# Optimization experiments

Measured on AMD Instinct MI355X. Metric: run time of the kernel, lower is better.

## Reference

```python
import jax, jax.numpy as jnp
import numpy as np

B, D, E, H, C = 2048, 1024, 8, 4096, 1024
TOP_K = 2
LN_EPS = 1e-5


def setup_inputs() -> dict:
    key = jax.random.key(0)
    ks = jax.random.split(key, 5)
    x = jax.random.normal(ks[0], (B, D), dtype=jnp.float32)
    Wr = jax.random.normal(ks[1], (D, E), dtype=jnp.float32) * 0.02
    br = jnp.zeros((E,), dtype=jnp.float32)
    ln_g = jnp.ones((E, D), dtype=jnp.float32)
    ln_b = jnp.zeros((E, D), dtype=jnp.float32)
    W1 = jax.random.normal(ks[2], (E, D, H), dtype=jnp.float32) * 0.02
    b1 = jnp.zeros((E, H), dtype=jnp.float32)
    W2 = jax.random.normal(ks[3], (E, H, C), dtype=jnp.float32) * 0.02
    b2 = jnp.zeros((E, C), dtype=jnp.float32)
    return {"x": x, "Wr": Wr, "br": br, "ln_g": ln_g, "ln_b": ln_b,
            "W1": W1, "b1": b1, "W2": W2, "b2": b2}


def reference(x, Wr, br, ln_g, ln_b, W1, b1, W2, b2):
    # Router (eval mode: no jitter)
    router_logits = x @ Wr + br                       # [B, E]
    topk_vals, topk_idx = jax.lax.top_k(router_logits, TOP_K)
    topk_w = jax.nn.softmax(topk_vals, axis=-1)       # [B, K]
    # Scatter top-k weights into a dense [B, E] combine matrix (indices unique per row)
    w_full = jnp.zeros((x.shape[0], E), dtype=x.dtype)
    w_full = w_full.at[jnp.arange(x.shape[0])[:, None], topk_idx].set(topk_w)
    # Shared LayerNorm statistics, per-expert affine
    mu = jnp.mean(x, axis=-1, keepdims=True)
    var = jnp.mean(jnp.square(x - mu), axis=-1, keepdims=True)
    xn = (x - mu) * jax.lax.rsqrt(var + LN_EPS)       # [B, D]
    xe = xn[:, None, :] * ln_g[None] + ln_b[None]     # [B, E, D]
    # Expert MLPs (dense over experts; combine weights zero-out non-selected experts)
    h = jax.nn.gelu(jnp.einsum('bed,edh->beh', xe, W1) + b1[None], approximate=False)
    y = jnp.einsum('beh,ehc->bec', h, W2) + b2[None]  # [B, E, C]
    out = jnp.einsum('be,bec->bc', w_full, y)         # weighted combine
    return out
```

## Files before the change

kernel.cpp:

```cpp
#include <hip/hip_runtime.h>
#include <hip/hip_bf16.h>

#define B_TOK 2048
#define D_DIM 1024
#define E_NUM 8
#define H_DIM 4096
#define C_DIM 1024
#define CAP   5120
#define MAXT  40

typedef __attribute__((ext_vector_type(8))) short bf16x8;
typedef __attribute__((ext_vector_type(4))) float floatx4;

__device__ __forceinline__ unsigned short f2bf(float f) {
  union { float f; unsigned int u; } a; a.f = f;
  unsigned int u = a.u;
  return (unsigned short)((u + 0x7FFFu + ((u >> 16) & 1u)) >> 16);
}

__device__ __forceinline__ void gload_lds16(const void* g, void* l) {
  __builtin_amdgcn_global_load_lds(
      (const __attribute__((address_space(1))) void*)g,
      (__attribute__((address_space(3))) void*)l, 16, 0, 0);
}

__global__ void kinit(int* counts) {
  if (threadIdx.x < E_NUM) counts[threadIdx.x] = 0;
}

__global__ __launch_bounds__(256) void krouter(const float* __restrict__ x,
                                               const float* __restrict__ Wr,
                                               const float* __restrict__ br,
                                               int2* meta_i, float4* meta_f, int* counts) {
  int b = blockIdx.x, t = threadIdx.x;
  const float4 xv = *(const float4*)(x + (size_t)b * D_DIM + t * 4);
  float v[10];
  v[0] = xv.x + xv.y + xv.z + xv.w;
  v[1] = xv.x * xv.x + xv.y * xv.y + xv.z * xv.z + xv.w * xv.w;
#pragma unroll
  for (int e = 0; e < 8; e++) v[2 + e] = 0.f;
  const float* wr = Wr + (size_t)(t * 4) * E_NUM;
  float xs[4] = {xv.x, xv.y, xv.z, xv.w};
#pragma unroll
  for (int j = 0; j < 4; j++) {
    float4 wa = *(const float4*)(wr + j * 8);
    float4 wb = *(const float4*)(wr + j * 8 + 4);
    v[2] += xs[j] * wa.x; v[3] += xs[j] * wa.y; v[4] += xs[j] * wa.z; v[5] += xs[j] * wa.w;
    v[6] += xs[j] * wb.x; v[7] += xs[j] * wb.y; v[8] += xs[j] * wb.z; v[9] += xs[j] * wb.w;
  }
#pragma unroll
  for (int i = 0; i < 10; i++) {
    float s = v[i];
#pragma unroll
    for (int off = 32; off > 0; off >>= 1) s += __shfl_down(s, off, 64);
    v[i] = s;
  }
  __shared__ float red[4][10];
  int lane = t & 63, wid = t >> 6;
  if (lane == 0) {
#pragma unroll
    for (int i = 0; i < 10; i++) red[wid][i] = v[i];
  }
  __syncthreads();
  if (t == 0) {
    float f[10];
#pragma unroll
    for (int i = 0; i < 10; i++) f[i] = red[0][i] + red[1][i] + red[2][i] + red[3][i];
    float mu = f[0] * (1.f / 1024.f);
    float var = f[1] * (1.f / 1024.f) - mu * mu;
    float rsig = rsqrtf(var + 1e-5f);
    float lg[8];
#pragma unroll
    for (int e = 0; e < 8; e++) lg[e] = f[2 + e] + br[e];
    int i0 = 0;
#pragma unroll
    for (int e = 1; e < 8; e++) if (lg[e] > lg[i0]) i0 = e;
    int i1 = (i0 == 0) ? 1 : 0;
#pragma unroll
    for (int e = 0; e < 8; e++) if (e != i0 && lg[e] > lg[i1]) i1 = e;
    float ex = expf(lg[i1] - lg[i0]);
    float w0 = 1.f / (1.f + ex);
    float w1 = 1.f - w0;
    atomicAdd(counts + i0, 1);
    atomicAdd(counts + i1, 1);
    meta_i[b] = make_int2(i0, i1);
    meta_f[b] = make_float4(w0, w1, mu, rsig);
  }
}

__global__ void kprefix(const int* counts, int* cursor, int* tmap_e, int* tmap_r) {
  if (threadIdx.x == 0) {
    int total = 0, tt = 0;
    for (int e = 0; e < E_NUM; e++) {
      cursor[e] = total;
      int nt = (counts[e] + 127) >> 7;
      for (int i = 0; i < nt; i++) { tmap_e[tt] = e; tmap_r[tt] = total + i * 128; tt++; }
      total += nt << 7;
    }
    for (; tt < MAXT; tt++) tmap_e[tt] = -1;
  }
}

__global__ __launch_bounds__(256) void kscatter(const float* __restrict__ x,
                                                const float* __restrict__ ln_g,
                                                const float* __restrict__ ln_b,
                                                const int2* __restrict__ meta_i,
                                                const float4* __restrict__ meta_f,
                                                int* cursor, int2* meta_s,
                                                unsigned short* __restrict__ xe) {
  int b = blockIdx.x, t = threadIdx.x;
  __shared__ int se[2], ss[2];
  __shared__ float smu, srs;
  if (t == 0) {
    int2 mi = meta_i[b];
    float4 mf = meta_f[b];
    int s0 = atomicAdd(cursor + mi.x, 1);
    int s1 = atomicAdd(cursor + mi.y, 1);
    meta_s[b] = make_int2(s0, s1);
    se[0] = mi.x; se[1] = mi.y; ss[0] = s0; ss[1] = s1;
    smu = mf.z; srs = mf.w;
  }
  __syncthreads();
  int i = t * 4;
  float4 xv = *(const float4*)(x + (size_t)b * D_DIM + i);
  float mu = smu, rs = srs;
  float xn0 = (xv.x - mu) * rs, xn1 = (xv.y - mu) * rs, xn2 = (xv.z - mu) * rs, xn3 = (xv.w - mu) * rs;
#pragma unroll
  for (int k = 0; k < 2; k++) {
    int e = se[k], s = ss[k];
    float4 g = *(const float4*)(ln_g + (size_t)e * D_DIM + i);
    float4 bb = *(const float4*)(ln_b + (size_t)e * D_DIM + i);
    union { unsigned short us[4]; uint2 v; } u;
    u.us[0] = f2bf(xn0 * g.x + bb.x);
    u.us[1] = f2bf(xn1 * g.y + bb.y);
    u.us[2] = f2bf(xn2 * g.z + bb.z);
    u.us[3] = f2bf(xn3 * g.w + bb.w);
    *(uint2*)(xe + (size_t)s * D_DIM + i) = u.v;
  }
}

__global__ __launch_bounds__(256) void ktranspose(const float* __restrict__ src,
                                                  unsigned short* __restrict__ dst,
                                                  int R, int C) {
  __shared__ float tile[64][65];
  int z = blockIdx.z;
  const float* s = src + (size_t)z * R * C;
  unsigned short* d = dst + (size_t)z * R * C;
  int cx = blockIdx.x * 64, ry = blockIdx.y * 64;
  int t = threadIdx.x;
  int cl4 = (t & 15) * 4, rl = t >> 4;
#pragma unroll
  for (int p = 0; p < 4; p++) {
    int r = rl + p * 16;
    float4 v = *(const float4*)(s + (size_t)(ry + r) * C + cx + cl4);
    tile[r][cl4] = v.x; tile[r][cl4 + 1] = v.y; tile[r][cl4 + 2] = v.z; tile[r][cl4 + 3] = v.w;
  }
  __syncthreads();
#pragma unroll
  for (int p = 0; p < 4; p++) {
    int c = rl + p * 16;
    union { unsigned short us[4]; uint2 v; } u;
    u.us[0] = f2bf(tile[cl4][c]);
    u.us[1] = f2bf(tile[cl4 + 1][c]);
    u.us[2] = f2bf(tile[cl4 + 2][c]);
    u.us[3] = f2bf(tile[cl4 + 3][c]);
    *(uint2*)(d + (size_t)(cx + c) * R + ry + cl4) = u.v;
  }
}

__global__ __launch_bounds__(256) void kgemm1(const unsigned short* __restrict__ xe,
                                              const unsigned short* __restrict__ w1t,
                                              const float* __restrict__ b1,
                                              unsigned short* __restrict__ h,
                                              const int* __restrict__ tmap_e,
                                              const int* __restrict__ tmap_r) {
  int e = tmap_e[blockIdx.y];
  if (e < 0) return;
  int row0 = tmap_r[blockIdx.y];
  int n0 = blockIdx.x * 128;
  const unsigned short* Ab = xe + (size_t)row0 * D_DIM;
  const unsigned short* Bb = w1t + (size_t)e * H_DIM * D_DIM + (size_t)n0 * D_DIM;
  __shared__ unsigned short As[128 * 32];
  __shared__ unsigned short Bs[128 * 32];
  int t = threadIdx.x, lane = t & 63, wid = t >> 6;
  int c0 = wid * 2, c1 = c0 + 1;
  int lr0 = c0 * 16 + (lane >> 2);
  int kc = (lane & 3) * 8;
  const unsigned short* ga0 = Ab + (size_t)lr0 * D_DIM + kc;
  const unsigned short* ga1 = ga0 + 16 * D_DIM;
  const unsigned short* gb0 = Bb + (size_t)lr0 * D_DIM + kc;
  const unsigned short* gb1 = gb0 + 16 * D_DIM;
  unsigned short* la0 = As + c0 * 512;
  unsigned short* la1 = As + c1 * 512;
  unsigned short* lb0 = Bs + c0 * 512;
  unsigned short* lb1 = Bs + c1 * 512;
  int l15 = lane & 15, q = lane >> 4;
  int wm = (wid & 1) * 64, wn = (wid >> 1) * 64;
  const unsigned short* pa[4];
  const unsigned short* pb[4];
#pragma unroll
  for (int i = 0; i < 4; i++) {
    pa[i] = As + (wm + i * 16 + l15) * 32 + q * 8;
    pb[i] = Bs + (wn + i * 16 + l15) * 32 + q * 8;
  }
  floatx4 acc[4][4];
#pragma unroll
  for (int i = 0; i < 4; i++)
#pragma unroll
    for (int j = 0; j < 4; j++) acc[i][j] = (floatx4){0.f, 0.f, 0.f, 0.f};

  for (int k0 = 0; k0 < D_DIM; k0 += 32) {
    gload_lds16(ga0, la0);
    gload_lds16(ga1, la1);
    gload_lds16(gb0, lb0);
    gload_lds16(gb1, lb1);
    __syncthreads();
    bf16x8 af[4], bfr[4];
#pragma unroll
    for (int i = 0; i < 4; i++) { af[i] = *(const bf16x8*)pa[i]; bfr[i] = *(const bf16x8*)pb[i]; }
#pragma unroll
    for (int mt = 0; mt < 4; mt++)
#pragma unroll
      for (int nt = 0; nt < 4; nt++)
        acc[mt][nt] = __builtin_amdgcn_mfma_f32_16x16x32_bf16(af[mt], bfr[nt], acc[mt][nt], 0, 0, 0);
    __syncthreads();
    ga0 += 32; ga1 += 32; gb0 += 32; gb1 += 32;
  }
  float b1v[4];
#pragma unroll
  for (int nt = 0; nt < 4; nt++) b1v[nt] = b1[(size_t)e * H_DIM + n0 + wn + nt * 16 + l15];
#pragma unroll
  for (int mt = 0; mt < 4; mt++) {
    int row = row0 + wm + mt * 16 + q * 4;
#pragma unroll
    for (int nt = 0; nt < 4; nt++) {
      int col = n0 + wn + nt * 16 + l15;
      unsigned short* hp = h + (size_t)row * H_DIM + col;
#pragma unroll
      for (int r = 0; r < 4; r++) {
        float v = acc[mt][nt][r] + b1v[nt];
        v = 0.5f * v * (1.f + erff(v * 0.70710678118f));
        hp[(size_t)r * H_DIM] = f2bf(v);
      }
    }
  }
}

__global__ __launch_bounds__(256) void kgemm2(const unsigned short* __restrict__ h,
                                              const unsigned short* __restrict__ w2t,
                                              float* __restrict__ ypart,
                                              const int* __restrict__ tmap_e,
                                              const int* __restrict__ tmap_r) {
  int e = tmap_e[blockIdx.y];
  if (e < 0) return;
  int row0 = tmap_r[blockIdx.y];
  int n0 = blockIdx.x * 128;
  int kz = blockIdx.z;
  const unsigned short* Ab = h + (size_t)row0 * H_DIM + kz * 2048;
  const unsigned short* Bb = w2t + (size_t)e * C_DIM * H_DIM + (size_t)n0 * H_DIM + kz * 2048;
  float* yo = ypart + (size_t)kz * CAP * C_DIM;
  __shared__ unsigned short As[128 * 32];
  __shared__ unsigned short Bs[128 * 32];
  int t = threadIdx.x, lane = t & 63, wid = t >> 6;
  int c0 = wid * 2, c1 = c0 + 1;
  int lr0 = c0 * 16 + (lane >> 2);
  int kc = (lane & 3) * 8;
  const unsigned short* ga0 = Ab + (size_t)lr0 * H_DIM + kc;
  const unsigned short* ga1 = ga0 + (size_t)16 * H_DIM;
  const unsigned short* gb0 = Bb + (size_t)lr0 * H_DIM + kc;
  const unsigned short* gb1 = gb0 + (size_t)16 * H_DIM;
  unsigned short* la0 = As + c0 * 512;
  unsigned short* la1 = As + c1 * 512;
  unsigned short* lb0 = Bs + c0 * 512;
  unsigned short* lb1 = Bs + c1 * 512;
  int l15 = lane & 15, q = lane >> 4;
  int wm = (wid & 1) * 64, wn = (wid >> 1) * 64;
  const unsigned short* pa[4];
  const unsigned short* pb[4];
#pragma unroll
  for (int i = 0; i < 4; i++) {
    pa[i] = As + (wm + i * 16 + l15) * 32 + q * 8;
    pb[i] = Bs + (wn + i * 16 + l15) * 32 + q * 8;
  }
  floatx4 acc[4][4];
#pragma unroll
  for (int i = 0; i < 4; i++)
#pragma unroll
    for (int j = 0; j < 4; j++) acc[i][j] = (floatx4){0.f, 0.f, 0.f, 0.f};

  for (int k0 = 0; k0 < 2048; k0 += 32) {
    gload_lds16(ga0, la0);
    gload_lds16(ga1, la1);
    gload_lds16(gb0, lb0);
    gload_lds16(gb1, lb1);
    __syncthreads();
    bf16x8 af[4], bfr[4];
#pragma unroll
    for (int i = 0; i < 4; i++) { af[i] = *(const bf16x8*)pa[i]; bfr[i] = *(const bf16x8*)pb[i]; }
#pragma unroll
    for (int mt = 0; mt < 4; mt++)
#pragma unroll
      for (int nt = 0; nt < 4; nt++)
        acc[mt][nt] = __builtin_amdgcn_mfma_f32_16x16x32_bf16(af[mt], bfr[nt], acc[mt][nt], 0, 0, 0);
    __syncthreads();
    ga0 += 32; ga1 += 32; gb0 += 32; gb1 += 32;
  }
#pragma unroll
  for (int mt = 0; mt < 4; mt++) {
    int rbase = row0 + wm + mt * 16 + q * 4;
#pragma unroll
    for (int nt = 0; nt < 4; nt++) {
      int col = n0 + wn + nt * 16 + l15;
#pragma unroll
      for (int r = 0; r < 4; r++)
        yo[(size_t)(rbase + r) * C_DIM + col] = acc[mt][nt][r];
    }
  }
}

__global__ __launch_bounds__(256) void kfinal(const float* __restrict__ ypart,
                                              const int2* __restrict__ meta_i,
                                              const int2* __restrict__ meta_s,
                                              const float4* __restrict__ meta_f,
                                              const float* __restrict__ b2,
                                              float* __restrict__ out) {
  int b = blockIdx.x, t = threadIdx.x;
  int i = t * 4;
  int2 mi = meta_i[b];
  int2 ms = meta_s[b];
  float4 mf = meta_f[b];
  const float* y0 = ypart;
  const float* y1 = ypart + (size_t)CAP * C_DIM;
  float4 a0 = *(const float4*)(y0 + (size_t)ms.x * C_DIM + i);
  float4 a1 = *(const float4*)(y1 + (size_t)ms.x * C_DIM + i);
  float4 c0 = *(const float4*)(y0 + (size_t)ms.y * C_DIM + i);
  float4 c1 = *(const float4*)(y1 + (size_t)ms.y * C_DIM + i);
  float4 p = *(const float4*)(b2 + (size_t)mi.x * C_DIM + i);
  float4 qv = *(const float4*)(b2 + (size_t)mi.y * C_DIM + i);
  float4 o;
  o.x = mf.x * (a0.x + a1.x + p.x) + mf.y * (c0.x + c1.x + qv.x);
  o.y = mf.x * (a0.y + a1.y + p.y) + mf.y * (c0.y + c1.y + qv.y);
  o.z = mf.x * (a0.z + a1.z + p.z) + mf.y * (c0.z + c1.z + qv.z);
  o.w = mf.x * (a0.w + a1.w + p.w) + mf.y * (c0.w + c1.w + qv.w);
  *(float4*)(out + (size_t)b * C_DIM + i) = o;
}

extern "C" void kernel_launch(void* const* d_in, const int* in_sizes, int n_in,
                              void* d_out, int out_size, void* d_ws, size_t ws_size,
                              hipStream_t stream) {
  const float* x    = (const float*)d_in[0];
  const float* Wr   = (const float*)d_in[1];
  const float* br   = (const float*)d_in[2];
  const float* ln_g = (const float*)d_in[3];
  const float* ln_b = (const float*)d_in[4];
  const float* W1   = (const float*)d_in[5];
  const float* b1   = (const float*)d_in[6];
  const float* W2   = (const float*)d_in[7];
  const float* b2   = (const float*)d_in[8];

  char* w = (char*)d_ws;
  auto alloc = [&](size_t sz) { char* p = w; w += (sz + 255) & ~(size_t)255; return p; };
  unsigned short* W1t = (unsigned short*)alloc((size_t)E_NUM * H_DIM * D_DIM * 2);
  unsigned short* W2t = (unsigned short*)alloc((size_t)E_NUM * C_DIM * H_DIM * 2);
  unsigned short* xe  = (unsigned short*)alloc((size_t)CAP * D_DIM * 2);
  unsigned short* hb  = (unsigned short*)alloc((size_t)CAP * H_DIM * 2);
  float* ypart        = (float*)alloc((size_t)2 * CAP * C_DIM * 4);
  int2* meta_i        = (int2*)alloc((size_t)B_TOK * 8);
  int2* meta_s        = (int2*)alloc((size_t)B_TOK * 8);
  float4* meta_f      = (float4*)alloc((size_t)B_TOK * 16);
  int* counts         = (int*)alloc(64);
  int* cursor         = (int*)alloc(64);
  int* tmap_e         = (int*)alloc(MAXT * 4);
  int* tmap_r         = (int*)alloc(MAXT * 4);

  hipLaunchKernelGGL(ktranspose, dim3(H_DIM / 64, D_DIM / 64, E_NUM), dim3(256), 0, stream,
                     W1, W1t, D_DIM, H_DIM);
  hipLaunchKernelGGL(ktranspose, dim3(C_DIM / 64, H_DIM / 64, E_NUM), dim3(256), 0, stream,
                     W2, W2t, H_DIM, C_DIM);
  hipLaunchKernelGGL(kinit, dim3(1), dim3(64), 0, stream, counts);
  hipLaunchKernelGGL(krouter, dim3(B_TOK), dim3(256), 0, stream,
                     x, Wr, br, meta_i, meta_f, counts);
  hipLaunchKernelGGL(kprefix, dim3(1), dim3(64), 0, stream,
                     counts, cursor, tmap_e, tmap_r);
  hipLaunchKernelGGL(kscatter, dim3(B_TOK), dim3(256), 0, stream,
                     x, ln_g, ln_b, meta_i, meta_f, cursor, meta_s, xe);
  hipLaunchKernelGGL(kgemm1, dim3(H_DIM / 128, MAXT), dim3(256), 0, stream,
                     xe, W1t, b1, hb, tmap_e, tmap_r);
  hipLaunchKernelGGL(kgemm2, dim3(C_DIM / 128, MAXT, 2), dim3(256), 0, stream,
                     hb, W2t, ypart, tmap_e, tmap_r);
  hipLaunchKernelGGL(kfinal, dim3(B_TOK), dim3(256), 0, stream,
                     ypart, meta_i, meta_s, meta_f, b2, (float*)d_out);
}
```

Before: 584.4 us.

## Double-buffer LDS tiles with BK=64 in both expert GEMM kernels

Both expert GEMM kernels now use a two-stage LDS ping-pong buffer with a 64-wide K tile instead of a single 32-wide tile. The next tile's global-to-LDS loads are issued right after one barrier per iteration, so they overlap with the MFMA work on the current tile. This removes the second barrier and halves the number of loop iterations. In exchange, LDS use per block grows to 64 KB, which can lower occupancy, and the 128-byte row stride may cause LDS bank conflicts.

```diff
diff --git a/kernel.cpp b/kernel.cpp
--- a/kernel.cpp
+++ b/kernel.cpp
@@ -168,6 +168,7 @@
   }
 }
 
+
 __global__ __launch_bounds__(256) void kgemm1(const unsigned short* __restrict__ xe,
                                               const unsigned short* __restrict__ w1t,
                                               const float* __restrict__ b1,
@@ -180,28 +181,28 @@
   int n0 = blockIdx.x * 128;
   const unsigned short* Ab = xe + (size_t)row0 * D_DIM;
   const unsigned short* Bb = w1t + (size_t)e * H_DIM * D_DIM + (size_t)n0 * D_DIM;
-  __shared__ unsigned short As[128 * 32];
-  __shared__ unsigned short Bs[128 * 32];
+  __shared__ unsigned short smem[32768];
+  unsigned short* As = smem;
+  unsigned short* Bs = smem + 16384;
   int t = threadIdx.x, lane = t & 63, wid = t >> 6;
-  int c0 = wid * 2, c1 = c0 + 1;
-  int lr0 = c0 * 16 + (lane >> 2);
-  int kc = (lane & 3) * 8;
-  const unsigned short* ga0 = Ab + (size_t)lr0 * D_DIM + kc;
-  const unsigned short* ga1 = ga0 + 16 * D_DIM;
-  const unsigned short* gb0 = Bb + (size_t)lr0 * D_DIM + kc;
-  const unsigned short* gb1 = gb0 + 16 * D_DIM;
-  unsigned short* la0 = As + c0 * 512;
-  unsigned short* la1 = As + c1 * 512;
-  unsigned short* lb0 = Bs + c0 * 512;
-  unsigned short* lb1 = Bs + c1 * 512;
+  int lrow = lane >> 3, kc = (lane & 7) * 8;
+  const unsigned short* ga[4];
+  const unsigned short* gb[4];
+  int lo[4];
+#pragma unroll
+  for (int j = 0; j < 4; j++) {
+    int r = wid * 32 + j * 8;
+    ga[j] = Ab + (size_t)(r + lrow) * D_DIM + kc;
+    gb[j] = Bb + (size_t)(r + lrow) * D_DIM + kc;
+    lo[j] = r * 64;
+  }
   int l15 = lane & 15, q = lane >> 4;
   int wm = (wid & 1) * 64, wn = (wid >> 1) * 64;
-  const unsigned short* pa[4];
-  const unsigned short* pb[4];
+  int paoff[4], pboff[4];
 #pragma unroll
   for (int i = 0; i < 4; i++) {
-    pa[i] = As + (wm + i * 16 + l15) * 32 + q * 8;
-    pb[i] = Bs + (wn + i * 16 + l15) * 32 + q * 8;
+    paoff[i] = (wm + i * 16 + l15) * 64 + q * 8;
+    pboff[i] = (wn + i * 16 + l15) * 64 + q * 8;
   }
   floatx4 acc[4][4];
 #pragma unroll
@@ -209,22 +210,39 @@
 #pragma unroll
     for (int j = 0; j < 4; j++) acc[i][j] = (floatx4){0.f, 0.f, 0.f, 0.f};
 
-  for (int k0 = 0; k0 < D_DIM; k0 += 32) {
-    gload_lds16(ga0, la0);
-    gload_lds16(ga1, la1);
-    gload_lds16(gb0, lb0);
-    gload_lds16(gb1, lb1);
+#pragma unroll
+  for (int j = 0; j < 4; j++) {
+    gload_lds16(ga[j], As + lo[j]);
+    gload_lds16(gb[j], Bs + lo[j]);
+    ga[j] += 64; gb[j] += 64;
+  }
+  const int NT = D_DIM / 64;
+  for (int kt = 0; kt < NT; kt++) {
+    int cur = (kt & 1) * 8192;
+    int nxt = 8192 - cur;
     __syncthreads();
-    bf16x8 af[4], bfr[4];
-#pragma unroll
-    for (int i = 0; i < 4; i++) { af[i] = *(const bf16x8*)pa[i]; bfr[i] = *(const bf16x8*)pb[i]; }
-#pragma unroll
-    for (int mt = 0; mt < 4; mt++)
-#pragma unroll
-      for (int nt = 0; nt < 4; nt++)
-        acc[mt][nt] = __builtin_amdgcn_mfma_f32_16x16x32_bf16(af[mt], bfr[nt], acc[mt][nt], 0, 0, 0);
-    __syncthreads();
-    ga0 += 32; ga1 += 32; gb0 += 32; gb1 += 32;
+    if (kt + 1 < NT) {
+#pragma unroll
+      for (int j = 0; j < 4; j++) {
+        gload_lds16(ga[j], As + nxt + lo[j]);
+        gload_lds16(gb[j], Bs + nxt + lo[j]);
+        ga[j] += 64; gb[j] += 64;
+      }
+    }
+#pragma unroll
+    for (int kk = 0; kk < 2; kk++) {
+      bf16x8 af[4], bfr[4];
+#pragma unroll
+      for (int i = 0; i < 4; i++) {
+        af[i]  = *(const bf16x8*)(As + cur + paoff[i] + kk * 32);
+        bfr[i] = *(const bf16x8*)(Bs + cur + pboff[i] + kk * 32);
+      }
+#pragma unroll
+      for (int mt = 0; mt < 4; mt++)
+#pragma unroll
+        for (int nt = 0; nt < 4; nt++)
+          acc[mt][nt] = __builtin_amdgcn_mfma_f32_16x16x32_bf16(af[mt], bfr[nt], acc[mt][nt], 0, 0, 0);
+    }
   }
   float b1v[4];
 #pragma unroll
@@ -259,28 +277,28 @@
   const unsigned short* Ab = h + (size_t)row0 * H_DIM + kz * 2048;
   const unsigned short* Bb = w2t + (size_t)e * C_DIM * H_DIM + (size_t)n0 * H_DIM + kz * 2048;
   float* yo = ypart + (size_t)kz * CAP * C_DIM;
-  __shared__ unsigned short As[128 * 32];
-  __shared__ unsigned short Bs[128 * 32];
+  __shared__ unsigned short smem[32768];
+  unsigned short* As = smem;
+  unsigned short* Bs = smem + 16384;
   int t = threadIdx.x, lane = t & 63, wid = t >> 6;
-  int c0 = wid * 2, c1 = c0 + 1;
-  int lr0 = c0 * 16 + (lane >> 2);
-  int kc = (lane & 3) * 8;
-  const unsigned short* ga0 = Ab + (size_t)lr0 * H_DIM + kc;
-  const unsigned short* ga1 = ga0 + (size_t)16 * H_DIM;
-  const unsigned short* gb0 = Bb + (size_t)lr0 * H_DIM + kc;
-  const unsigned short* gb1 = gb0 + (size_t)16 * H_DIM;
-  unsigned short* la0 = As + c0 * 512;
-  unsigned short* la1 = As + c1 * 512;
-  unsigned short* lb0 = Bs + c0 * 512;
-  unsigned short* lb1 = Bs + c1 * 512;
+  int lrow = lane >> 3, kc = (lane & 7) * 8;
+  const unsigned short* ga[4];
+  const unsigned short* gb[4];
+  int lo[4];
+#pragma unroll
+  for (int j = 0; j < 4; j++) {
+    int r = wid * 32 + j * 8;
+    ga[j] = Ab + (size_t)(r + lrow) * H_DIM + kc;
+    gb[j] = Bb + (size_t)(r + lrow) * H_DIM + kc;
+    lo[j] = r * 64;
+  }
   int l15 = lane & 15, q = lane >> 4;
   int wm = (wid & 1) * 64, wn = (wid >> 1) * 64;
-  const unsigned short* pa[4];
-  const unsigned short* pb[4];
+  int paoff[4], pboff[4];
 #pragma unroll
   for (int i = 0; i < 4; i++) {
-    pa[i] = As + (wm + i * 16 + l15) * 32 + q * 8;
-    pb[i] = Bs + (wn + i * 16 + l15) * 32 + q * 8;
+    paoff[i] = (wm + i * 16 + l15) * 64 + q * 8;
+    pboff[i] = (wn + i * 16 + l15) * 64 + q * 8;
   }
   floatx4 acc[4][4];
 #pragma unroll
@@ -288,22 +306,39 @@
 #pragma unroll
     for (int j = 0; j < 4; j++) acc[i][j] = (floatx4){0.f, 0.f, 0.f, 0.f};
 
-  for (int k0 = 0; k0 < 2048; k0 += 32) {
-    gload_lds16(ga0, la0);
-    gload_lds16(ga1, la1);
-    gload_lds16(gb0, lb0);
-    gload_lds16(gb1, lb1);
+#pragma unroll
+  for (int j = 0; j < 4; j++) {
+    gload_lds16(ga[j], As + lo[j]);
+    gload_lds16(gb[j], Bs + lo[j]);
+    ga[j] += 64; gb[j] += 64;
+  }
+  const int NT = 2048 / 64;
+  for (int kt = 0; kt < NT; kt++) {
+    int cur = (kt & 1) * 8192;
+    int nxt = 8192 - cur;
     __syncthreads();
-    bf16x8 af[4], bfr[4];
-#pragma unroll
-    for (int i = 0; i < 4; i++) { af[i] = *(const bf16x8*)pa[i]; bfr[i] = *(const bf16x8*)pb[i]; }
-#pragma unroll
-    for (int mt = 0; mt < 4; mt++)
-#pragma unroll
-      for (int nt = 0; nt < 4; nt++)
-        acc[mt][nt] = __builtin_amdgcn_mfma_f32_16x16x32_bf16(af[mt], bfr[nt], acc[mt][nt], 0, 0, 0);
-    __syncthreads();
-    ga0 += 32; ga1 += 32; gb0 += 32; gb1 += 32;
+    if (kt + 1 < NT) {
+#pragma unroll
+      for (int j = 0; j < 4; j++) {
+        gload_lds16(ga[j], As + nxt + lo[j]);
+        gload_lds16(gb[j], Bs + nxt + lo[j]);
+        ga[j] += 64; gb[j] += 64;
+      }
+    }
+#pragma unroll
+    for (int kk = 0; kk < 2; kk++) {
+      bf16x8 af[4], bfr[4];
+#pragma unroll
+      for (int i = 0; i < 4; i++) {
+        af[i]  = *(const bf16x8*)(As + cur + paoff[i] + kk * 32);
+        bfr[i] = *(const bf16x8*)(Bs + cur + pboff[i] + kk * 32);
+      }
+#pragma unroll
+      for (int mt = 0; mt < 4; mt++)
+#pragma unroll
+        for (int nt = 0; nt < 4; nt++)
+          acc[mt][nt] = __builtin_amdgcn_mfma_f32_16x16x32_bf16(af[mt], bfr[nt], acc[mt][nt], 0, 0, 0);
+    }
   }
 #pragma unroll
   for (int mt = 0; mt < 4; mt++) {
```

Result: no change. 578.0 us (-1.1%).
